# Optimization experiments

Measured on AMD Instinct MI355X. Metric: run time of the kernel, lower is better.

Reference implementation:

```python
import jax, jax.numpy as jnp
import numpy as np

B, HEADS, HEAD_DIM, WS = 64, 6, 32, 8
POS_DIM = 12  # (dim//4)//4 = 192//16
N = WS ** 3


def _ln(x, g, b, eps=1e-5):
    mu = jnp.mean(x, axis=-1, keepdims=True)
    var = jnp.var(x, axis=-1, keepdims=True)
    return (x - mu) / jnp.sqrt(var + eps) * g + b


def setup_inputs() -> dict:
    key = jax.random.key(0)
    ks = jax.random.split(key, 10)
    s = 0.02
    inp = {
        'q': jax.random.normal(ks[0], (B, HEADS, N, HEAD_DIM), jnp.float32),
        'k': jax.random.normal(ks[1], (B, HEADS, N, HEAD_DIM), jnp.float32),
        'v': jax.random.normal(ks[2], (B, HEADS, N, HEAD_DIM), jnp.float32),
        'h': WS, 'w': WS, 'd': WS,
        'pos_proj_w': jax.random.normal(ks[3], (3, POS_DIM), jnp.float32) * s,
        'pos_proj_b': jnp.zeros((POS_DIM,), jnp.float32),
        'ln1_g': jnp.ones((POS_DIM,), jnp.float32),
        'ln1_b': jnp.zeros((POS_DIM,), jnp.float32),
        'w1': jax.random.normal(ks[4], (POS_DIM, POS_DIM), jnp.float32) * s,
        'b1': jnp.zeros((POS_DIM,), jnp.float32),
        'ln2_g': jnp.ones((POS_DIM,), jnp.float32),
        'ln2_b': jnp.zeros((POS_DIM,), jnp.float32),
        'w2': jax.random.normal(ks[5], (POS_DIM, POS_DIM), jnp.float32) * s,
        'b2': jnp.zeros((POS_DIM,), jnp.float32),
        'ln3_g': jnp.ones((POS_DIM,), jnp.float32),
        'ln3_b': jnp.zeros((POS_DIM,), jnp.float32),
        'w3': jax.random.normal(ks[6], (POS_DIM, HEADS), jnp.float32) * s,
        'b3': jnp.zeros((HEADS,), jnp.float32),
    }
    return inp


def reference(q, k, v, h, w, d,
              pos_proj_w, pos_proj_b,
              ln1_g, ln1_b, w1, b1,
              ln2_g, ln2_b, w2, b2,
              ln3_g, ln3_b, w3, b3):
    scale = HEAD_DIM ** (-0.5)
    attn = jnp.einsum('bhnc,bhmc->bhnm', q * scale, k)

    # candidate relative offsets table: ((2h-1)(2w-1)(2d-1), 3)
    bh = jnp.arange(1 - h, h, dtype=jnp.float32)
    bw = jnp.arange(1 - w, w, dtype=jnp.float32)
    bd = jnp.arange(1 - d, d, dtype=jnp.float32)
    biases = jnp.stack(jnp.meshgrid(bh, bw, bd, indexing='ij')).reshape(3, -1).T

    # per-pair relative index (faithfully sums the 3 shifted coords, as source does)
    coords = jnp.stack(jnp.meshgrid(jnp.arange(h), jnp.arange(w), jnp.arange(d),
                                    indexing='ij')).reshape(3, -1)  # (3, N)
    rel = coords[:, :, None] - coords[:, None, :]  # (3, N, N)
    rel_idx = (rel[0] + h - 1) + (rel[1] + w - 1) + (rel[2] + d - 1)  # (N, N)

    # dynamic pos-bias MLP
    x = biases @ pos_proj_w + pos_proj_b
    x = jax.nn.relu(_ln(x, ln1_g, ln1_b)) @ w1 + b1
    x = jax.nn.relu(_ln(x, ln2_g, ln2_b)) @ w2 + b2
    pos = jax.nn.relu(_ln(x, ln3_g, ln3_b)) @ w3 + b3  # (table, heads)

    rpb = pos[rel_idx]                       # (N, N, heads) gather
    attn = attn + jnp.transpose(rpb, (2, 0, 1))[None]  # (1, heads, N, N)

    attn = jax.nn.softmax(attn, axis=-1)
    return jnp.einsum('bhnm,bhmc->bhnc', attn, v)
```

## Files before the change

### kernel.cpp

```cpp
#include <hip/hip_runtime.h>
#include <math.h>

typedef _Float16 h8 __attribute__((ext_vector_type(8)));
typedef _Float16 h4 __attribute__((ext_vector_type(4)));
typedef float    f4 __attribute__((ext_vector_type(4)));

#define NHEADS 6
#define HDIM   32
#define NTOK   512
#define NTAB   43
#define LOG2E  1.44269504088896340736f

#define FRAG_BYTES (64L * NHEADS * 32 * 64 * 8 * 2)
#define OFF_Q 4096L
#define OFF_K (OFF_Q + FRAG_BYTES)
#define OFF_V (OFF_K + FRAG_BYTES)

__device__ inline int ds3(int x) {
  return (x >> 6) + ((x >> 3) & 7) + (x & 7);
}

__device__ inline void ln_relu12(const float* x, float* t, const float* g, const float* b) {
  float mu = 0.f;
#pragma unroll
  for (int j = 0; j < 12; j++) mu += x[j];
  mu *= (1.f / 12.f);
  float var = 0.f;
#pragma unroll
  for (int j = 0; j < 12; j++) { float d = x[j] - mu; var += d * d; }
  var *= (1.f / 12.f);
  float inv = rsqrtf(var + 1e-5f);
#pragma unroll
  for (int j = 0; j < 12; j++) {
    float y = (x[j] - mu) * inv * g[j] + b[j];
    t[j] = y > 0.f ? y : 0.f;
  }
}

__device__ inline void mm12(const float* t, float* x, const float* w, const float* c) {
#pragma unroll
  for (int j = 0; j < 12; j++) {
    float acc = c[j];
#pragma unroll
    for (int i = 0; i < 12; i++) acc += t[i] * w[i * 12 + j];
    x[j] = acc;
  }
}

__global__ __launch_bounds__(256)
void prepack_kernel(const float* __restrict__ q, const float* __restrict__ k,
                    const float* __restrict__ v, _Float16* __restrict__ Qf,
                    _Float16* __restrict__ Kf, _Float16* __restrict__ Vf,
                    const float* __restrict__ pw, const float* __restrict__ pb,
                    const float* __restrict__ g1, const float* __restrict__ b1,
                    const float* __restrict__ w1, const float* __restrict__ c1,
                    const float* __restrict__ g2, const float* __restrict__ b2,
                    const float* __restrict__ w2, const float* __restrict__ c2,
                    const float* __restrict__ g3, const float* __restrict__ b3,
                    const float* __restrict__ w3, const float* __restrict__ c3,
                    float* __restrict__ posb)
{
  __shared__ _Float16 Qs[64 * 40];
  __shared__ _Float16 Ks[64 * 40];
  __shared__ _Float16 Vt[32 * 72];

  const float SC = 0.17677669529663687f * LOG2E;
  const int tid = threadIdx.x;

  if (blockIdx.x == 0 && blockIdx.y == 0 && blockIdx.z == 0 && tid < NTAB) {
    const float bh_ = -7.0f;
    const float bw_ = (float)(tid / 15) - 7.0f;
    const float bd_ = (float)(tid % 15) - 7.0f;
    float x[12], t[12];
#pragma unroll
    for (int j = 0; j < 12; j++)
      x[j] = bh_ * pw[j] + bw_ * pw[12 + j] + bd_ * pw[24 + j] + pb[j];
    ln_relu12(x, t, g1, b1); mm12(t, x, w1, c1);
    ln_relu12(x, t, g2, b2); mm12(t, x, w2, c2);
    ln_relu12(x, t, g3, b3);
#pragma unroll
    for (int hd = 0; hd < NHEADS; hd++) {
      float acc = c3[hd];
#pragma unroll
      for (int i = 0; i < 12; i++) acc += t[i] * w3[i * NHEADS + hd];
      posb[tid * NHEADS + hd] = acc * LOG2E;
    }
  }

  const int c   = blockIdx.x;
  const int bh  = blockIdx.z * NHEADS + blockIdx.y;
  const long base = (long)bh * NTOK * HDIM + (long)c * 64 * HDIM;
  const float4* qg = (const float4*)(q + base);
  const float4* kg = (const float4*)(k + base);
  const float4* vg = (const float4*)(v + base);

#pragma unroll
  for (int i = 0; i < 2; i++) {
    int f = i * 256 + tid;
    int row = f >> 3, c4 = f & 7;
    float4 a = qg[f];
    h4 ah = { (_Float16)(a.x * SC), (_Float16)(a.y * SC),
              (_Float16)(a.z * SC), (_Float16)(a.w * SC) };
    *(h4*)&Qs[row * 40 + c4 * 4] = ah;
    float4 e = kg[f];
    h4 eh = { (_Float16)e.x, (_Float16)e.y, (_Float16)e.z, (_Float16)e.w };
    *(h4*)&Ks[row * 40 + c4 * 4] = eh;
    float4 w = vg[f];
    Vt[(c4 * 4 + 0) * 72 + row] = (_Float16)w.x;
    Vt[(c4 * 4 + 1) * 72 + row] = (_Float16)w.y;
    Vt[(c4 * 4 + 2) * 72 + row] = (_Float16)w.z;
    Vt[(c4 * 4 + 3) * 72 + row] = (_Float16)w.w;
  }
  __syncthreads();

  const int lane = tid & 63, t = tid >> 6;
  const int quad = lane >> 4, l16 = lane & 15;
  const long fo = ((long)(bh * 32 + c * 4 + t) * 64 + lane) * 8;

  *(h8*)(Qf + fo) = *(const h8*)&Qs[(t * 16 + l16) * 40 + quad * 8];
  *(h8*)(Kf + fo) = *(const h8*)&Ks[(t * 16 + l16) * 40 + quad * 8];
  *(h8*)(Vf + fo) = *(const h8*)&Vt[((t & 1) * 16 + l16) * 72 + (t >> 1) * 32 + quad * 8];
}

__global__ __launch_bounds__(256, 4)
void attn_kernel(const _Float16* __restrict__ Qf, const _Float16* __restrict__ Kf,
                 const _Float16* __restrict__ Vf, const float* __restrict__ posb,
                 float* __restrict__ out)
{
  __shared__ __align__(16) char smem[4][2][2304];
  __shared__ f4 posw4r[NTAB];

  const int tid  = threadIdx.x;
  const int wave = tid >> 6;
  const int lane = tid & 63;
  const int quad = lane >> 4;
  const int l16  = lane & 15;
  const int bh   = blockIdx.x;
  const int h    = bh % NHEADS;
  const int qq   = blockIdx.y;

  if (tid >= 3 && tid < NTAB) {
    f4 pv = { posb[tid * NHEADS + h],       posb[(tid - 1) * NHEADS + h],
              posb[(tid - 2) * NHEADS + h], posb[(tid - 3) * NHEADS + h] };
    posw4r[tid] = pv;
  }
  __syncthreads();

  int qt[2] = { qq * 8 + wave * 2, qq * 8 + wave * 2 + 1 };
  h8 qf[2];
  int qs21[2];
#pragma unroll
  for (int ti = 0; ti < 2; ti++) {
    qf[ti] = *(const h8*)(Qf + ((long)(bh * 32 + qt[ti]) * 64 + lane) * 8);
    qs21[ti] = ds3(qt[ti] * 16) + (l16 >> 3) + (l16 & 7) + 21;
  }
  const int kdq = (quad >> 1) + (quad & 1) * 4;

  f4 o[2][2];
#pragma unroll
  for (int ti = 0; ti < 2; ti++) { o[ti][0] = f4{0,0,0,0}; o[ti][1] = f4{0,0,0,0}; }
  float lp[2] = {0.f, 0.f};

  const _Float16* kbase = Kf + ((long)bh * 32 * 64 + lane) * 8;
  const _Float16* vbase = Vf + ((long)bh * 32 * 64 + lane) * 8;

#pragma unroll
  for (int kc = 0; kc < 8; kc++) {
    h8 kf[4], vf[4];
#pragma unroll
    for (int t = 0; t < 4; t++) {
      kf[t] = *(const h8*)(kbase + (kc * 4 + t) * 64 * 8);
      vf[t] = *(const h8*)(vbase + (kc * 4 + t) * 64 * 8);
    }

#pragma unroll
    for (int ti = 0; ti < 2; ti++) {
      _Float16* pt = (_Float16*)smem[wave][ti];
      f4 s[4];
#pragma unroll
      for (int t = 0; t < 4; t++) {
        int idx0 = qs21[ti] - (kc + t * 2 + kdq);
        f4 cin = posw4r[idx0];
        s[t] = __builtin_amdgcn_mfma_f32_16x16x32_f16(kf[t], qf[ti], cin, 0, 0, 0);
      }
#pragma unroll
      for (int t = 0; t < 4; t++) {
        float p0 = __builtin_amdgcn_exp2f(s[t][0]);
        float p1 = __builtin_amdgcn_exp2f(s[t][1]);
        float p2 = __builtin_amdgcn_exp2f(s[t][2]);
        float p3 = __builtin_amdgcn_exp2f(s[t][3]);
        lp[ti] += (p0 + p1) + (p2 + p3);
        h4 hv = { (_Float16)p0, (_Float16)p1, (_Float16)p2, (_Float16)p3 };
        *(h4*)&pt[l16 * 72 + t * 16 + quad * 4] = hv;
      }
#pragma unroll
      for (int kt = 0; kt < 2; kt++) {
        h8 pf = *(const h8*)&pt[l16 * 72 + kt * 32 + quad * 8];
        o[ti][0] = __builtin_amdgcn_mfma_f32_16x16x32_f16(vf[kt * 2 + 0], pf, o[ti][0], 0, 0, 0);
        o[ti][1] = __builtin_amdgcn_mfma_f32_16x16x32_f16(vf[kt * 2 + 1], pf, o[ti][1], 0, 0, 0);
      }
    }
  }

#pragma unroll
  for (int ti = 0; ti < 2; ti++) {
    float l = lp[ti];
    l += __shfl_xor(l, 16);
    l += __shfl_xor(l, 32);
    const float inv = 1.f / l;
    float* os = (float*)smem[wave][ti];
    f4 w0 = { o[ti][0][0] * inv, o[ti][0][1] * inv, o[ti][0][2] * inv, o[ti][0][3] * inv };
    f4 w1 = { o[ti][1][0] * inv, o[ti][1][1] * inv, o[ti][1][2] * inv, o[ti][1][3] * inv };
    *(f4*)&os[l16 * 36 + quad * 4]      = w0;
    *(f4*)&os[l16 * 36 + 16 + quad * 4] = w1;
    const int q_ = lane >> 2, seg = lane & 3;
    f4 r0 = *(const f4*)&os[q_ * 36 + seg * 8];
    f4 r1 = *(const f4*)&os[q_ * 36 + seg * 8 + 4];
    float* orow = out + (long)bh * NTOK * HDIM + (long)(qt[ti] * 16 + q_) * HDIM + seg * 8;
    *(float4*)orow       = *(float4*)&r0;
    *(float4*)(orow + 4) = *(float4*)&r1;
  }
}

extern "C" void kernel_launch(void* const* d_in, const int* in_sizes, int n_in,
                              void* d_out, int out_size, void* d_ws, size_t ws_size,
                              hipStream_t stream) {
  (void)in_sizes; (void)n_in; (void)out_size; (void)ws_size;
  const float* q  = (const float*)d_in[0];
  const float* k  = (const float*)d_in[1];
  const float* v  = (const float*)d_in[2];
  const float* pw  = (const float*)d_in[6];
  const float* pb  = (const float*)d_in[7];
  const float* g1  = (const float*)d_in[8];
  const float* b1  = (const float*)d_in[9];
  const float* w1  = (const float*)d_in[10];
  const float* c1  = (const float*)d_in[11];
  const float* g2  = (const float*)d_in[12];
  const float* b2  = (const float*)d_in[13];
  const float* w2  = (const float*)d_in[14];
  const float* c2  = (const float*)d_in[15];
  const float* g3  = (const float*)d_in[16];
  const float* b3  = (const float*)d_in[17];
  const float* w3  = (const float*)d_in[18];
  const float* c3  = (const float*)d_in[19];

  char* ws = (char*)d_ws;
  float*     posb = (float*)ws;
  _Float16*  Qf   = (_Float16*)(ws + OFF_Q);
  _Float16*  Kf   = (_Float16*)(ws + OFF_K);
  _Float16*  Vf   = (_Float16*)(ws + OFF_V);
  float* outp = (float*)d_out;

  prepack_kernel<<<dim3(8, NHEADS, 64), 256, 0, stream>>>(
      q, k, v, Qf, Kf, Vf,
      pw, pb, g1, b1, w1, c1, g2, b2, w2, c2, g3, b3, w3, c3, posb);
  attn_kernel<<<dim3(384, 4), 256, 0, stream>>>(Qf, Kf, Vf, posb, outp);
}
```

Baseline: 165.2 us.

## Fuse prepack into attention kernel with double-buffered LDS staging of K/V

Removes the separate prepack kernel and fp16 fragment workspace; the attention kernel now computes the positional-bias table per block, converts Q from fp32 in registers, and loads fp32 K/V into double-buffered LDS tiles with a one-chunk register prefetch. This aims to remove the extra launch and workspace round-trip. In exchange, each block redundantly reads fp32 K/V for its head and recomputes the small MLP, and adds per-chunk barriers.

```diff
diff --git a/kernel.cpp b/kernel.cpp
--- a/kernel.cpp
+++ b/kernel.cpp
@@ -11,11 +11,6 @@
 #define NTAB   43
 #define LOG2E  1.44269504088896340736f
 
-#define FRAG_BYTES (64L * NHEADS * 32 * 64 * 8 * 2)
-#define OFF_Q 4096L
-#define OFF_K (OFF_Q + FRAG_BYTES)
-#define OFF_V (OFF_K + FRAG_BYTES)
-
 __device__ inline int ds3(int x) {
   return (x >> 6) + ((x >> 3) & 7) + (x & 7);
 }
@@ -47,88 +42,23 @@
   }
 }
 
-__global__ __launch_bounds__(256)
-void prepack_kernel(const float* __restrict__ q, const float* __restrict__ k,
-                    const float* __restrict__ v, _Float16* __restrict__ Qf,
-                    _Float16* __restrict__ Kf, _Float16* __restrict__ Vf,
-                    const float* __restrict__ pw, const float* __restrict__ pb,
-                    const float* __restrict__ g1, const float* __restrict__ b1,
-                    const float* __restrict__ w1, const float* __restrict__ c1,
-                    const float* __restrict__ g2, const float* __restrict__ b2,
-                    const float* __restrict__ w2, const float* __restrict__ c2,
-                    const float* __restrict__ g3, const float* __restrict__ b3,
-                    const float* __restrict__ w3, const float* __restrict__ c3,
-                    float* __restrict__ posb)
-{
-  __shared__ _Float16 Qs[64 * 40];
-  __shared__ _Float16 Ks[64 * 40];
-  __shared__ _Float16 Vt[32 * 72];
-
-  const float SC = 0.17677669529663687f * LOG2E;
-  const int tid = threadIdx.x;
-
-  if (blockIdx.x == 0 && blockIdx.y == 0 && blockIdx.z == 0 && tid < NTAB) {
-    const float bh_ = -7.0f;
-    const float bw_ = (float)(tid / 15) - 7.0f;
-    const float bd_ = (float)(tid % 15) - 7.0f;
-    float x[12], t[12];
-#pragma unroll
-    for (int j = 0; j < 12; j++)
-      x[j] = bh_ * pw[j] + bw_ * pw[12 + j] + bd_ * pw[24 + j] + pb[j];
-    ln_relu12(x, t, g1, b1); mm12(t, x, w1, c1);
-    ln_relu12(x, t, g2, b2); mm12(t, x, w2, c2);
-    ln_relu12(x, t, g3, b3);
-#pragma unroll
-    for (int hd = 0; hd < NHEADS; hd++) {
-      float acc = c3[hd];
-#pragma unroll
-      for (int i = 0; i < 12; i++) acc += t[i] * w3[i * NHEADS + hd];
-      posb[tid * NHEADS + hd] = acc * LOG2E;
-    }
-  }
-
-  const int c   = blockIdx.x;
-  const int bh  = blockIdx.z * NHEADS + blockIdx.y;
-  const long base = (long)bh * NTOK * HDIM + (long)c * 64 * HDIM;
-  const float4* qg = (const float4*)(q + base);
-  const float4* kg = (const float4*)(k + base);
-  const float4* vg = (const float4*)(v + base);
-
-#pragma unroll
-  for (int i = 0; i < 2; i++) {
-    int f = i * 256 + tid;
-    int row = f >> 3, c4 = f & 7;
-    float4 a = qg[f];
-    h4 ah = { (_Float16)(a.x * SC), (_Float16)(a.y * SC),
-              (_Float16)(a.z * SC), (_Float16)(a.w * SC) };
-    *(h4*)&Qs[row * 40 + c4 * 4] = ah;
-    float4 e = kg[f];
-    h4 eh = { (_Float16)e.x, (_Float16)e.y, (_Float16)e.z, (_Float16)e.w };
-    *(h4*)&Ks[row * 40 + c4 * 4] = eh;
-    float4 w = vg[f];
-    Vt[(c4 * 4 + 0) * 72 + row] = (_Float16)w.x;
-    Vt[(c4 * 4 + 1) * 72 + row] = (_Float16)w.y;
-    Vt[(c4 * 4 + 2) * 72 + row] = (_Float16)w.z;
-    Vt[(c4 * 4 + 3) * 72 + row] = (_Float16)w.w;
-  }
-  __syncthreads();
-
-  const int lane = tid & 63, t = tid >> 6;
-  const int quad = lane >> 4, l16 = lane & 15;
-  const long fo = ((long)(bh * 32 + c * 4 + t) * 64 + lane) * 8;
-
-  *(h8*)(Qf + fo) = *(const h8*)&Qs[(t * 16 + l16) * 40 + quad * 8];
-  *(h8*)(Kf + fo) = *(const h8*)&Ks[(t * 16 + l16) * 40 + quad * 8];
-  *(h8*)(Vf + fo) = *(const h8*)&Vt[((t & 1) * 16 + l16) * 72 + (t >> 1) * 32 + quad * 8];
-}
-
 __global__ __launch_bounds__(256, 4)
-void attn_kernel(const _Float16* __restrict__ Qf, const _Float16* __restrict__ Kf,
-                 const _Float16* __restrict__ Vf, const float* __restrict__ posb,
-                 float* __restrict__ out)
+void fused_attn_kernel(const float* __restrict__ q, const float* __restrict__ k,
+                       const float* __restrict__ v,
+                       const float* __restrict__ pw, const float* __restrict__ pb,
+                       const float* __restrict__ g1, const float* __restrict__ b1,
+                       const float* __restrict__ w1, const float* __restrict__ c1,
+                       const float* __restrict__ g2, const float* __restrict__ b2,
+                       const float* __restrict__ w2, const float* __restrict__ c2,
+                       const float* __restrict__ g3, const float* __restrict__ b3,
+                       const float* __restrict__ w3, const float* __restrict__ c3,
+                       float* __restrict__ out)
 {
   __shared__ __align__(16) char smem[4][2][2304];
   __shared__ f4 posw4r[NTAB];
+  __shared__ float posb_s[NTAB * NHEADS];
+  __shared__ __align__(16) _Float16 Ks[2][64 * 40];
+  __shared__ __align__(16) _Float16 Vt[2][32 * 72];
 
   const int tid  = threadIdx.x;
   const int wave = tid >> 6;
@@ -138,20 +68,65 @@
   const int bh   = blockIdx.x;
   const int h    = bh % NHEADS;
   const int qq   = blockIdx.y;
+  const float SC = 0.17677669529663687f * LOG2E;
+
+  const long bhbase = (long)bh * NTOK * HDIM;
+  const float4* kg = (const float4*)(k + bhbase);
+  const float4* vg = (const float4*)(v + bhbase);
+
+  if (tid < NTAB) {
+    const float bh_ = -7.0f;
+    const float bw_ = (float)(tid / 15) - 7.0f;
+    const float bd_ = (float)(tid % 15) - 7.0f;
+    float x[12], t[12];
+#pragma unroll
+    for (int j = 0; j < 12; j++)
+      x[j] = bh_ * pw[j] + bw_ * pw[12 + j] + bd_ * pw[24 + j] + pb[j];
+    ln_relu12(x, t, g1, b1); mm12(t, x, w1, c1);
+    ln_relu12(x, t, g2, b2); mm12(t, x, w2, c2);
+    ln_relu12(x, t, g3, b3);
+#pragma unroll
+    for (int hd = 0; hd < NHEADS; hd++) {
+      float acc = c3[hd];
+#pragma unroll
+      for (int i = 0; i < 12; i++) acc += t[i] * w3[i * NHEADS + hd];
+      posb_s[tid * NHEADS + hd] = acc * LOG2E;
+    }
+  }
+
+#pragma unroll
+  for (int i = 0; i < 2; i++) {
+    int f = i * 256 + tid, row = f >> 3, c4 = f & 7;
+    float4 e = kg[f];
+    h4 eh = { (_Float16)e.x, (_Float16)e.y, (_Float16)e.z, (_Float16)e.w };
+    *(h4*)&Ks[0][row * 40 + c4 * 4] = eh;
+    float4 w = vg[f];
+    Vt[0][(c4 * 4 + 0) * 72 + row] = (_Float16)w.x;
+    Vt[0][(c4 * 4 + 1) * 72 + row] = (_Float16)w.y;
+    Vt[0][(c4 * 4 + 2) * 72 + row] = (_Float16)w.z;
+    Vt[0][(c4 * 4 + 3) * 72 + row] = (_Float16)w.w;
+  }
+  __syncthreads();
 
   if (tid >= 3 && tid < NTAB) {
-    f4 pv = { posb[tid * NHEADS + h],       posb[(tid - 1) * NHEADS + h],
-              posb[(tid - 2) * NHEADS + h], posb[(tid - 3) * NHEADS + h] };
+    f4 pv = { posb_s[tid * NHEADS + h],       posb_s[(tid - 1) * NHEADS + h],
+              posb_s[(tid - 2) * NHEADS + h], posb_s[(tid - 3) * NHEADS + h] };
     posw4r[tid] = pv;
   }
-  __syncthreads();
 
   int qt[2] = { qq * 8 + wave * 2, qq * 8 + wave * 2 + 1 };
   h8 qf[2];
   int qs21[2];
 #pragma unroll
   for (int ti = 0; ti < 2; ti++) {
-    qf[ti] = *(const h8*)(Qf + ((long)(bh * 32 + qt[ti]) * 64 + lane) * 8);
+    const float* qrow = q + bhbase + (long)(qt[ti] * 16 + l16) * HDIM + quad * 8;
+    float4 a = *(const float4*)qrow;
+    float4 b = *(const float4*)(qrow + 4);
+    h8 qh = { (_Float16)(a.x * SC), (_Float16)(a.y * SC),
+              (_Float16)(a.z * SC), (_Float16)(a.w * SC),
+              (_Float16)(b.x * SC), (_Float16)(b.y * SC),
+              (_Float16)(b.z * SC), (_Float16)(b.w * SC) };
+    qf[ti] = qh;
     qs21[ti] = ds3(qt[ti] * 16) + (l16 >> 3) + (l16 & 7) + 21;
   }
   const int kdq = (quad >> 1) + (quad & 1) * 4;
@@ -161,16 +136,24 @@
   for (int ti = 0; ti < 2; ti++) { o[ti][0] = f4{0,0,0,0}; o[ti][1] = f4{0,0,0,0}; }
   float lp[2] = {0.f, 0.f};
 
-  const _Float16* kbase = Kf + ((long)bh * 32 * 64 + lane) * 8;
-  const _Float16* vbase = Vf + ((long)bh * 32 * 64 + lane) * 8;
-
-#pragma unroll
+  __syncthreads();
+
+#pragma unroll 2
   for (int kc = 0; kc < 8; kc++) {
+    const int cur = kc & 1;
+
+    float4 kreg0, kreg1, vreg0, vreg1;
+    if (kc < 7) {
+      const int fb = (kc + 1) * 512 + tid;
+      kreg0 = kg[fb];       kreg1 = kg[fb + 256];
+      vreg0 = vg[fb];       vreg1 = vg[fb + 256];
+    }
+
     h8 kf[4], vf[4];
 #pragma unroll
     for (int t = 0; t < 4; t++) {
-      kf[t] = *(const h8*)(kbase + (kc * 4 + t) * 64 * 8);
-      vf[t] = *(const h8*)(vbase + (kc * 4 + t) * 64 * 8);
+      kf[t] = *(const h8*)&Ks[cur][(t * 16 + l16) * 40 + quad * 8];
+      vf[t] = *(const h8*)&Vt[cur][((t & 1) * 16 + l16) * 72 + (t >> 1) * 32 + quad * 8];
     }
 
 #pragma unroll
@@ -199,6 +182,23 @@
         o[ti][0] = __builtin_amdgcn_mfma_f32_16x16x32_f16(vf[kt * 2 + 0], pf, o[ti][0], 0, 0, 0);
         o[ti][1] = __builtin_amdgcn_mfma_f32_16x16x32_f16(vf[kt * 2 + 1], pf, o[ti][1], 0, 0, 0);
       }
+    }
+
+    if (kc < 7) {
+      const int nb = cur ^ 1;
+#pragma unroll
+      for (int i = 0; i < 2; i++) {
+        float4 e = (i == 0) ? kreg0 : kreg1;
+        float4 w = (i == 0) ? vreg0 : vreg1;
+        int f = i * 256 + tid, row = f >> 3, c4 = f & 7;
+        h4 eh = { (_Float16)e.x, (_Float16)e.y, (_Float16)e.z, (_Float16)e.w };
+        *(h4*)&Ks[nb][row * 40 + c4 * 4] = eh;
+        Vt[nb][(c4 * 4 + 0) * 72 + row] = (_Float16)w.x;
+        Vt[nb][(c4 * 4 + 1) * 72 + row] = (_Float16)w.y;
+        Vt[nb][(c4 * 4 + 2) * 72 + row] = (_Float16)w.z;
+        Vt[nb][(c4 * 4 + 3) * 72 + row] = (_Float16)w.w;
+      }
+      __syncthreads();
     }
   }
 
@@ -225,7 +225,7 @@
 extern "C" void kernel_launch(void* const* d_in, const int* in_sizes, int n_in,
                               void* d_out, int out_size, void* d_ws, size_t ws_size,
                               hipStream_t stream) {
-  (void)in_sizes; (void)n_in; (void)out_size; (void)ws_size;
+  (void)in_sizes; (void)n_in; (void)out_size; (void)d_ws; (void)ws_size;
   const float* q  = (const float*)d_in[0];
   const float* k  = (const float*)d_in[1];
   const float* v  = (const float*)d_in[2];
@@ -243,16 +243,9 @@
   const float* b3  = (const float*)d_in[17];
   const float* w3  = (const float*)d_in[18];
   const float* c3  = (const float*)d_in[19];
-
-  char* ws = (char*)d_ws;
-  float*     posb = (float*)ws;
-  _Float16*  Qf   = (_Float16*)(ws + OFF_Q);
-  _Float16*  Kf   = (_Float16*)(ws + OFF_K);
-  _Float16*  Vf   = (_Float16*)(ws + OFF_V);
   float* outp = (float*)d_out;
 
-  prepack_kernel<<<dim3(8, NHEADS, 64), 256, 0, stream>>>(
-      q, k, v, Qf, Kf, Vf,
-      pw, pb, g1, b1, w1, c1, g2, b2, w2, c2, g3, b3, w3, c3, posb);
-  attn_kernel<<<dim3(384, 4), 256, 0, stream>>>(Qf, Kf, Vf, posb, outp);
-}
+  fused_attn_kernel<<<dim3(384, 4), 256, 0, stream>>>(
+      q, k, v,
+      pw, pb, g1, b1, w1, c1, g2, b2, w2, c2, g3, b3, w3, c3, outp);
+}
```

Measured after the change: 249.0 us. 50.7% more time.
